# Kernel tuning notes

Hardware: AMD Instinct MI355X
Metric: run time of the kernel (lower is better)

## Reference

```python
import jax, jax.numpy as jnp
import numpy as np

HEADS = 8
DIM_HEAD = 64
DIM = 512
SCALE = DIM ** -0.5  # NOTE: original scales by dim**-0.5, not dim_head**-0.5


def setup_inputs() -> dict:
    key = jax.random.key(0)
    k1, k2, k3 = jax.random.split(key, 3)
    b, n = 2, 4096
    x = jax.random.normal(k1, (b, n, DIM), dtype=jnp.float32)
    Wqkv = jax.random.normal(k2, (DIM, 3 * HEADS * DIM_HEAD), dtype=jnp.float32) * (DIM ** -0.5)
    Wout = jax.random.normal(k3, (HEADS * DIM_HEAD, DIM), dtype=jnp.float32) * ((HEADS * DIM_HEAD) ** -0.5)
    b_out = jnp.zeros((DIM,), dtype=jnp.float32)
    return {"x": x, "Wqkv": Wqkv, "Wout": Wout, "b_out": b_out}


def reference(x, Wqkv, Wout, b_out):
    b, n, _ = x.shape
    h, d = HEADS, DIM_HEAD
    qkv = x @ Wqkv  # [b, n, 3*h*d]
    q, k, v = jnp.split(qkv, 3, axis=-1)
    to_heads = lambda t: t.reshape(b, n, h, d).transpose(0, 2, 1, 3)  # [b,h,n,d]
    q, k, v = to_heads(q), to_heads(k), to_heads(v)
    half = n // 2
    q_s, q_t = q[:, :, :half], q[:, :, half:]
    k_t = k[:, :, half:]  # k_s is unused in the original module
    v_s, v_t = v[:, :, :half], v[:, :, half:]
    # temporal branch: q_t attends to k_t, reads v_t
    dots_t = jnp.einsum('bhid,bhjd->bhij', q_t, k_t) * SCALE
    # spatial branch: cross-term q_s attends to k_t, reads v_s
    dots_s = jnp.einsum('bhid,bhjd->bhij', q_s, k_t) * SCALE
    attn_s = jax.nn.softmax(dots_s, axis=-1)
    attn_t = jax.nn.softmax(dots_t, axis=-1)
    out_s = jnp.einsum('bhij,bhjd->bhid', attn_s, v_s)
    out_t = jnp.einsum('bhij,bhjd->bhid', attn_t, v_t)
    out = jnp.concatenate([out_s, out_t], axis=2)  # [b,h,n,d]
    out = out.transpose(0, 2, 1, 3).reshape(b, n, h * d)
    return out @ Wout + b_out
```

## Files before the change

### kernel.cpp

```cpp
#include <hip/hip_runtime.h>
#include <hip/hip_bf16.h>

typedef __bf16 bf16;
typedef _Float16 f16;
typedef __bf16 bf16x4 __attribute__((ext_vector_type(4)));
typedef __bf16 bf16x8 __attribute__((ext_vector_type(8)));
typedef _Float16 f16x2 __attribute__((ext_vector_type(2)));
typedef _Float16 f16x4 __attribute__((ext_vector_type(4)));
typedef _Float16 f16x8 __attribute__((ext_vector_type(8)));
typedef float floatx4 __attribute__((ext_vector_type(4)));

static __device__ __forceinline__ floatx4 mfma_bf16(bf16x8 a, bf16x8 b, floatx4 c) {
  return __builtin_amdgcn_mfma_f32_16x16x32_bf16(a, b, c, 0, 0, 0);
}
static __device__ __forceinline__ floatx4 mfma_f16k32(f16x8 a, f16x8 b, floatx4 c) {
  return __builtin_amdgcn_mfma_f32_16x16x32_f16(a, b, c, 0, 0, 0);
}

static __device__ __forceinline__ void async16(void* lds, const void* gp) {
  __builtin_amdgcn_global_load_lds(
      (const __attribute__((address_space(1))) void*)gp,
      (__attribute__((address_space(3))) void*)lds, 16, 0, 0);
}

static __device__ __forceinline__ bf16x8 cvt8(float4 f0, float4 f1) {
  bf16x8 r;
  r[0] = (bf16)f0.x; r[1] = (bf16)f0.y; r[2] = (bf16)f0.z; r[3] = (bf16)f0.w;
  r[4] = (bf16)f1.x; r[5] = (bf16)f1.y; r[6] = (bf16)f1.z; r[7] = (bf16)f1.w;
  return r;
}

#define HEADS 8
#define DIMH 64
#define DIM 512
#define SEQ 4096
#define HALF 2048
#define BATCH 2
#define MROWS (BATCH * SEQ)
#define ELEMS ((size_t)MROWS * DIM)
#define NPARTS 4

#define C2F (0.044194173824159216f * 1.4426950408889634f)

__global__ __launch_bounds__(256)
void prep(const float* __restrict__ X, bf16* __restrict__ Xb,
          const float* __restrict__ wqkv, bf16* __restrict__ W1t,
          const float* __restrict__ wout, bf16* __restrict__ W2t) {
  __shared__ float tile[32][33];
  const int bid = blockIdx.x, t = threadIdx.x;
  if (bid < 2048) {
    size_t i = ((size_t)bid * 256 + t) * 8;
    float4 f0 = *reinterpret_cast<const float4*>(X + i);
    float4 f1 = *reinterpret_cast<const float4*>(X + i + 4);
    *reinterpret_cast<bf16x8*>(Xb + i) = cvt8(f0, f1);
    return;
  }
  const float* src; bf16* dst; int N, id;
  if (bid < 2816) { id = bid - 2048; src = wqkv; dst = W1t; N = 1536; }
  else            { id = bid - 2816; src = wout; dst = W2t; N = 512; }
  const int nb = N / 32;
  const int n0 = (id % nb) * 32, k0 = (id / nb) * 32;
  const int r = t >> 3, c4 = (t & 7) * 4;
  float4 v = *reinterpret_cast<const float4*>(src + (size_t)(k0 + r) * N + n0 + c4);
  tile[r][c4 + 0] = v.x; tile[r][c4 + 1] = v.y;
  tile[r][c4 + 2] = v.z; tile[r][c4 + 3] = v.w;
  __syncthreads();
  bf16x4 o;
#pragma unroll
  for (int i = 0; i < 4; ++i) o[i] = (bf16)tile[c4 + i][r];
  *reinterpret_cast<bf16x4*>(dst + (size_t)(n0 + r) * DIM + k0 + c4) = o;
}

__global__ __launch_bounds__(256)
void qkv_gemm(const bf16* __restrict__ Xb, const bf16* __restrict__ Wt,
              bf16* __restrict__ Qw, bf16* __restrict__ Kw, f16* __restrict__ Vt) {
  __shared__ __align__(16) char smem_raw[36864];

  const int m0 = blockIdx.x * 128, n0 = blockIdx.y * 128;
  const int t = threadIdx.x;
  const int wave = t >> 6, lane = t & 63, quad = lane >> 4, l16 = lane & 15;
  const int wr = wave >> 1, wc = wave & 1;

  f16 (*Ts)[72] = (f16(*)[72])(smem_raw + wave * 9216);

  floatx4 acc[4][4] = {};

  auto issue = [&](int buf, int k0) {
    bf16* Asf = (bf16*)(smem_raw + buf * 16384);
    bf16* Bsf = Asf + 4096;
#pragma unroll
    for (int it = 0; it < 2; ++it) {
      int g = it * 256 + t, row = g >> 2, c8 = (g & 3) * 8;
      async16(Asf + (size_t)g * 8, Xb + (size_t)(m0 + row) * DIM + k0 + c8);
      async16(Bsf + (size_t)g * 8, Wt + (size_t)(n0 + row) * DIM + k0 + c8);
    }
  };

  issue(0, 0);
  int buf = 0;
#pragma unroll 1
  for (int k0 = 0; k0 < DIM; k0 += 32) {
    __syncthreads();
    if (k0 + 32 < DIM) issue(buf ^ 1, k0 + 32);

    const bf16* Asf = (const bf16*)(smem_raw + buf * 16384);
    const bf16* Bsf = Asf + 4096;
    bf16x8 af[4], bfr[4];
#pragma unroll
    for (int mi = 0; mi < 4; ++mi)
      af[mi] = *reinterpret_cast<const bf16x8*>(
          Asf + (size_t)(wr * 64 + mi * 16 + l16) * 32 + quad * 8);
#pragma unroll
    for (int ni = 0; ni < 4; ++ni)
      bfr[ni] = *reinterpret_cast<const bf16x8*>(
          Bsf + (size_t)(wc * 64 + ni * 16 + l16) * 32 + quad * 8);
#pragma unroll
    for (int mi = 0; mi < 4; ++mi)
#pragma unroll
      for (int ni = 0; ni < 4; ++ni)
        acc[mi][ni] = mfma_bf16(af[mi], bfr[ni], acc[mi][ni]);
    buf ^= 1;
  }

  if (n0 < 1024) {
#pragma unroll
    for (int mi = 0; mi < 4; ++mi)
#pragma unroll
      for (int ni = 0; ni < 4; ++ni)
#pragma unroll
        for (int r = 0; r < 4; ++r) {
          int row = m0 + wr * 64 + mi * 16 + quad * 4 + r;
          int col = n0 + wc * 64 + ni * 16 + l16;
          int which = col >> 9, cc = col & 511;
          int head = cc >> 6, dim = cc & 63;
          int bb = row >> 12, nn = row & 4095;
          float val = acc[mi][ni][r];
          if (which == 0) val *= C2F;
          bf16* dst = which ? Kw : Qw;
          dst[(((size_t)(bb * HEADS + head)) * SEQ + nn) * DIMH + dim] = (bf16)val;
        }
  } else {
    __syncthreads();
    int head = (n0 + wc * 64 - 1024) >> 6;
#pragma unroll
    for (int mi = 0; mi < 4; ++mi)
#pragma unroll
      for (int ni = 0; ni < 4; ++ni) {
        f16x4 pv;
#pragma unroll
        for (int r = 0; r < 4; ++r) pv[r] = (f16)acc[mi][ni][r];
        *reinterpret_cast<f16x4*>(&Ts[ni * 16 + l16][mi * 16 + quad * 4]) = pv;
      }
    int bb = m0 >> 12, nnb = (m0 + wr * 64) & 4095;
    size_t base = ((size_t)(bb * HEADS + head)) * DIMH;
#pragma unroll
    for (int it = 0; it < 8; ++it) {
      int idx = lane + it * 64;
      int d = idx >> 3, ns = (idx & 7) * 8;
      *reinterpret_cast<f16x8*>(Vt + (base + d) * SEQ + nnb + ns) =
          *reinterpret_cast<const f16x8*>(&Ts[d][ns]);
    }
  }
}

__global__ __launch_bounds__(256)
void attn_kernel(const bf16* __restrict__ Q, const bf16* __restrict__ K,
                 const f16* __restrict__ Vt, f16* __restrict__ Opart,
                 float* __restrict__ Lpart) {
  __shared__ __align__(16) char smem[32768];

  const int bid = blockIdx.x;
  const int xcd = bid & 7, rem = bid >> 3;
  const int qt = rem & 31, ghi = rem >> 5;
  const int g = ghi * 8 + xcd;
  const int h = g >> 3, z = g & 7;
  const int bb = z >> 2, part = z & 3;

  const int t = threadIdx.x;
  const int wave = t >> 6, lane = t & 63, quad = lane >> 4, l16 = lane & 15;

  const size_t hb = ((size_t)(bb * HEADS + h)) * SEQ * DIMH;
  const int vhalf = (qt < 16) ? 0 : HALF;
  const int kstart = HALF + part * 512;
  const int vstart = vhalf + part * 512;
  const int q0 = qt * 128 + wave * 32;

  bf16x8 qa[2][2];
#pragma unroll
  for (int mt = 0; mt < 2; ++mt)
#pragma unroll
    for (int kc = 0; kc < 2; ++kc)
      qa[mt][kc] = *reinterpret_cast<const bf16x8*>(
          Q + hb + (size_t)(q0 + mt * 16 + l16) * DIMH + kc * 32 + quad * 8);

  floatx4 o_acc[2][4] = {};
  float l_acc[2] = {0.f, 0.f};

  const int r = t >> 3;
  const int rr = r & 15;
  const int kappa = (rr >> 2) * 8 + (rr & 3) + ((r & 16) ? 4 : 0);
  const int kchunk = (t & 7) ^ (r & 7);
  const bf16* kSrc = K + hb + (size_t)(kstart + kappa) * DIMH + kchunk * 8;

  const int vd = t >> 2;
  const int vchunk = (t & 3) ^ ((vd >> 1) & 3);
  const f16* vSrc = Vt + hb + (size_t)vd * SEQ + vstart + vchunk * 8;

  auto issue = [&](int slot, int kc0) {
    async16(smem + slot * 8192 + t * 16, kSrc + (size_t)kc0 * DIMH);
    async16(smem + slot * 8192 + 4096 + t * 16, vSrc + kc0);
  };

  const int koffA = l16 * 128 + ((quad ^ (l16 & 7)) * 16);
  const int voff = l16 * 64 + ((quad ^ ((l16 >> 1) & 3)) * 16);

  auto compute = [&](const char* Kb) {
    const char* Vb = Kb + 4096;
    __builtin_amdgcn_s_setprio(1);
    bf16x8 kaA0 = *reinterpret_cast<const bf16x8*>(Kb + koffA);
    bf16x8 kaA1 = *reinterpret_cast<const bf16x8*>(Kb + (koffA ^ 64));
    bf16x8 kaB0 = *reinterpret_cast<const bf16x8*>(Kb + 2048 + koffA);
    bf16x8 kaB1 = *reinterpret_cast<const bf16x8*>(Kb + 2048 + (koffA ^ 64));

    f16x8 pbm[2];
#pragma unroll
    for (int mt = 0; mt < 2; ++mt) {
      floatx4 stA = {0.f, 0.f, 0.f, 0.f}, stB = {0.f, 0.f, 0.f, 0.f};
      stA = mfma_bf16(kaA0, qa[mt][0], stA);
      stA = mfma_bf16(kaA1, qa[mt][1], stA);
      stB = mfma_bf16(kaB0, qa[mt][0], stB);
      stB = mfma_bf16(kaB1, qa[mt][1], stB);
      float ls = l_acc[mt];
      f16x8 pb;
#pragma unroll
      for (int rr2 = 0; rr2 < 4; ++rr2) {
        float pA = __builtin_amdgcn_exp2f(stA[rr2]);
        float pB = __builtin_amdgcn_exp2f(stB[rr2]);
        ls += pA + pB;
        pb[rr2] = (f16)pA;
        pb[4 + rr2] = (f16)pB;
      }
      l_acc[mt] = ls;
      pbm[mt] = pb;
    }
#pragma unroll
    for (int dsub = 0; dsub < 4; ++dsub) {
      f16x8 va = *reinterpret_cast<const f16x8*>(Vb + voff + dsub * 1024);
      o_acc[0][dsub] = mfma_f16k32(va, pbm[0], o_acc[0][dsub]);
      o_acc[1][dsub] = mfma_f16k32(va, pbm[1], o_acc[1][dsub]);
    }
    __builtin_amdgcn_s_setprio(0);
  };

  issue(0, 0);
  issue(1, 32);
  issue(2, 64);
#pragma unroll 1
  for (int i = 0; i < 16; ++i) {
    if (i <= 13)      asm volatile("s_waitcnt vmcnt(4)" ::: "memory");
    else if (i == 14) asm volatile("s_waitcnt vmcnt(2)" ::: "memory");
    else              asm volatile("s_waitcnt vmcnt(0)" ::: "memory");
    asm volatile("s_barrier" ::: "memory");
    if (i <= 12) issue((i + 3) & 3, (i + 3) * 32);
    compute(smem + (i & 3) * 8192);
  }

  f16* Op = Opart + (size_t)part * ELEMS;
  float* Lp = Lpart + (size_t)part * MROWS * HEADS;
#pragma unroll
  for (int mt = 0; mt < 2; ++mt) {
    float v = l_acc[mt];
    v += __shfl_xor(v, 16);
    v += __shfl_xor(v, 32);
    int n = q0 + mt * 16 + l16;
    size_t rowidx = (size_t)(bb * SEQ + n);
    if (quad == 0) Lp[rowidx * HEADS + h] = v;
    size_t rowbase = rowidx * DIM + h * DIMH;
#pragma unroll
    for (int dsub = 0; dsub < 4; ++dsub) {
      f16x4 ov;
#pragma unroll
      for (int r2 = 0; r2 < 4; ++r2) ov[r2] = (f16)o_acc[mt][dsub][r2];
      *reinterpret_cast<f16x4*>(Op + rowbase + dsub * 16 + quad * 4) = ov;
    }
  }
}

__global__ __launch_bounds__(256)
void out_gemm(const f16* __restrict__ Opart, const float* __restrict__ Lpart,
              const bf16* __restrict__ Wt, const float* __restrict__ bias,
              float* __restrict__ out) {
  __shared__ __align__(16) bf16 Asf[64 * 64];
  __shared__ __align__(16) bf16 Bsf[64 * 64];

  const int m0 = blockIdx.x * 64, n0 = blockIdx.y * 64;
  const int t = threadIdx.x;
  const int wave = t >> 6, lane = t & 63, quad = lane >> 4, l16 = lane & 15;
  const int m_off = (wave >> 1) * 32, n_off = (wave & 1) * 32;

  int srowi[2], sc8[2];
#pragma unroll
  for (int it = 0; it < 2; ++it) {
    int g = t + it * 256;
    srowi[it] = g >> 3; sc8[it] = (g & 7) * 8;
  }

  float linv[2][8];
#pragma unroll
  for (int it = 0; it < 2; ++it) {
    size_t ar = (size_t)(m0 + srowi[it]);
#pragma unroll
    for (int hh = 0; hh < 8; ++hh) {
      float s = 0.f;
#pragma unroll
      for (int p = 0; p < NPARTS; ++p)
        s += Lpart[(size_t)p * MROWS * HEADS + ar * HEADS + hh];
      linv[it][hh] = 1.0f / s;
    }
  }

  floatx4 acc[2][2] = {};

  f16x8 oreg[2][NPARTS];
  auto loadO = [&](int k0) {
#pragma unroll
    for (int it = 0; it < 2; ++it) {
      size_t abase = (size_t)(m0 + srowi[it]) * DIM + k0 + sc8[it];
#pragma unroll
      for (int p = 0; p < NPARTS; ++p)
        oreg[it][p] = *reinterpret_cast<const f16x8*>(Opart + (size_t)p * ELEMS + abase);
    }
  };

  loadO(0);
#pragma unroll 1
  for (int k0 = 0; k0 < DIM; k0 += 64) {
#pragma unroll
    for (int it = 0; it < 2; ++it) {
      int g = t + it * 256;
      async16(Bsf + (size_t)g * 8, Wt + (size_t)(n0 + srowi[it]) * DIM + k0 + sc8[it]);
      float inv = linv[it][(k0 + sc8[it]) >> 6];
      bf16x8 a;
#pragma unroll
      for (int j = 0; j < 8; ++j)
        a[j] = (bf16)(((float)oreg[it][0][j] + (float)oreg[it][1][j] +
                       (float)oreg[it][2][j] + (float)oreg[it][3][j]) * inv);
      *reinterpret_cast<bf16x8*>(Asf + (size_t)g * 8) = a;
    }
    __syncthreads();
    int nk = k0 + 64; if (nk >= DIM) nk = 0;
    loadO(nk);

#pragma unroll
    for (int kk = 0; kk < 2; ++kk) {
      bf16x8 a0 = *reinterpret_cast<const bf16x8*>(Asf + (size_t)(m_off + l16) * 64 + kk * 32 + quad * 8);
      bf16x8 a1 = *reinterpret_cast<const bf16x8*>(Asf + (size_t)(m_off + 16 + l16) * 64 + kk * 32 + quad * 8);
      bf16x8 b0 = *reinterpret_cast<const bf16x8*>(Bsf + (size_t)(n_off + l16) * 64 + kk * 32 + quad * 8);
      bf16x8 b1 = *reinterpret_cast<const bf16x8*>(Bsf + (size_t)(n_off + 16 + l16) * 64 + kk * 32 + quad * 8);
      acc[0][0] = mfma_bf16(a0, b0, acc[0][0]);
      acc[0][1] = mfma_bf16(a0, b1, acc[0][1]);
      acc[1][0] = mfma_bf16(a1, b0, acc[1][0]);
      acc[1][1] = mfma_bf16(a1, b1, acc[1][1]);
    }
    __syncthreads();
  }

#pragma unroll
  for (int mi = 0; mi < 2; ++mi)
#pragma unroll
    for (int ni = 0; ni < 2; ++ni)
#pragma unroll
      for (int r = 0; r < 4; ++r) {
        int row = m0 + m_off + mi * 16 + quad * 4 + r;
        int col = n0 + n_off + ni * 16 + l16;
        out[(size_t)row * DIM + col] = acc[mi][ni][r] + bias[col];
      }
}

extern "C" void kernel_launch(void* const* d_in, const int* in_sizes, int n_in,
                              void* d_out, int out_size, void* d_ws, size_t ws_size,
                              hipStream_t stream) {
  const float* x = (const float*)d_in[0];
  const float* wqkv = (const float*)d_in[1];
  const float* wout = (const float*)d_in[2];
  const float* bout = (const float*)d_in[3];
  float* out = (float*)d_out;

  char* ws = (char*)d_ws;
  f16* Opart = (f16*)ws;
  bf16* Xb = (bf16*)ws;
  bf16* Qw = (bf16*)(ws + ((size_t)32 << 20));
  bf16* Kw = Qw + ELEMS;
  f16* Vt = (f16*)(Kw + ELEMS);
  bf16* WtQKV = (bf16*)(Vt + ELEMS);
  bf16* WtOUT = WtQKV + (size_t)1536 * 512;
  float* Lpart = (float*)(WtOUT + (size_t)512 * 512);

  prep<<<3072, 256, 0, stream>>>(x, Xb, wqkv, WtQKV, wout, WtOUT);
  qkv_gemm<<<dim3(MROWS / 128, 1536 / 128), 256, 0, stream>>>(Xb, WtQKV, Qw, Kw, Vt);
  attn_kernel<<<2048, 256, 0, stream>>>(Qw, Kw, Vt, Opart, Lpart);
  out_gemm<<<dim3(MROWS / 64, DIM / 64), 256, 0, stream>>>(Opart, Lpart, WtOUT, bout, out);
}
```

Before: 156.2 us.

## Split attention into single-wave blocks with barrier-free double buffering and MFMA row sums

The attention kernel now runs one wave per block (8192 blocks of 64 threads) instead of four waves sharing K/V tiles. Each wave loads its own K/V tiles through a two-slot buffer and no longer needs s_barrier. The softmax row sum is computed by an MFMA against a ones vector in place of scalar adds and cross-lane shuffles. Dropping the barrier and the shuffles cuts synchronisation and VALU work, at the cost of four times the K/V global-to-LDS traffic, since tiles are no longer shared across waves, and a shallower prefetch depth.

Result: slower. 170.1 us (+8.9%).

```diff
diff --git a/kernel.cpp b/kernel.cpp
--- a/kernel.cpp
+++ b/kernel.cpp
@@ -163,27 +163,27 @@
   }
 }
 
-__global__ __launch_bounds__(256)
+__global__ __launch_bounds__(64, 4)
 void attn_kernel(const bf16* __restrict__ Q, const bf16* __restrict__ K,
                  const f16* __restrict__ Vt, f16* __restrict__ Opart,
                  float* __restrict__ Lpart) {
-  __shared__ __align__(16) char smem[32768];
+  __shared__ __align__(16) char smem[16384];
 
   const int bid = blockIdx.x;
   const int xcd = bid & 7, rem = bid >> 3;
-  const int qt = rem & 31, ghi = rem >> 5;
+  const int qw = rem & 127, ghi = rem >> 7;
   const int g = ghi * 8 + xcd;
   const int h = g >> 3, z = g & 7;
   const int bb = z >> 2, part = z & 3;
 
   const int t = threadIdx.x;
-  const int wave = t >> 6, lane = t & 63, quad = lane >> 4, l16 = lane & 15;
+  const int quad = t >> 4, l16 = t & 15;
 
   const size_t hb = ((size_t)(bb * HEADS + h)) * SEQ * DIMH;
-  const int vhalf = (qt < 16) ? 0 : HALF;
+  const int vhalf = (qw < 64) ? 0 : HALF;
   const int kstart = HALF + part * 512;
   const int vstart = vhalf + part * 512;
-  const int q0 = qt * 128 + wave * 32;
+  const int q0 = qw * 32;
 
   bf16x8 qa[2][2];
 #pragma unroll
@@ -194,25 +194,39 @@
           Q + hb + (size_t)(q0 + mt * 16 + l16) * DIMH + kc * 32 + quad * 8);
 
   floatx4 o_acc[2][4] = {};
-  float l_acc[2] = {0.f, 0.f};
-
-  const int r = t >> 3;
-  const int rr = r & 15;
-  const int kappa = (rr >> 2) * 8 + (rr & 3) + ((r & 16) ? 4 : 0);
-  const int kchunk = (t & 7) ^ (r & 7);
-  const bf16* kSrc = K + hb + (size_t)(kstart + kappa) * DIMH + kchunk * 8;
-
-  const int vd = t >> 2;
-  const int vchunk = (t & 3) ^ ((vd >> 1) & 3);
-  const f16* vSrc = Vt + hb + (size_t)vd * SEQ + vstart + vchunk * 8;
+  floatx4 lacc[2] = {};
+
+  const bf16* kSrcIt[4];
+#pragma unroll
+  for (int it = 0; it < 4; ++it) {
+    int g256 = it * 64 + t;
+    int r = g256 >> 3;
+    int rr = r & 15;
+    int kappa = (rr >> 2) * 8 + (rr & 3) + ((r & 16) ? 4 : 0);
+    int kchunk = (g256 & 7) ^ (r & 7);
+    kSrcIt[it] = K + hb + (size_t)(kstart + kappa) * DIMH + kchunk * 8;
+  }
+  const int vd0 = t >> 2;
+  const int vchunk = (t & 3) ^ ((vd0 >> 1) & 3);
+  const f16* vSrc = Vt + hb + (size_t)vd0 * SEQ + vstart + vchunk * 8;
 
   auto issue = [&](int slot, int kc0) {
-    async16(smem + slot * 8192 + t * 16, kSrc + (size_t)kc0 * DIMH);
-    async16(smem + slot * 8192 + 4096 + t * 16, vSrc + kc0);
+#pragma unroll
+    for (int it = 0; it < 4; ++it)
+      async16(smem + slot * 8192 + it * 1024 + t * 16,
+              kSrcIt[it] + (size_t)kc0 * DIMH);
+#pragma unroll
+    for (int it = 0; it < 4; ++it)
+      async16(smem + slot * 8192 + 4096 + it * 1024 + t * 16,
+              vSrc + kc0 + (size_t)(it * 16) * SEQ);
   };
 
   const int koffA = l16 * 128 + ((quad ^ (l16 & 7)) * 16);
   const int voff = l16 * 64 + ((quad ^ ((l16 >> 1) & 3)) * 16);
+
+  f16x8 ones;
+#pragma unroll
+  for (int j = 0; j < 8; ++j) ones[j] = (f16)1.0f;
 
   auto compute = [&](const char* Kb) {
     const char* Vb = Kb + 4096;
@@ -230,18 +244,14 @@
       stA = mfma_bf16(kaA1, qa[mt][1], stA);
       stB = mfma_bf16(kaB0, qa[mt][0], stB);
       stB = mfma_bf16(kaB1, qa[mt][1], stB);
-      float ls = l_acc[mt];
       f16x8 pb;
 #pragma unroll
       for (int rr2 = 0; rr2 < 4; ++rr2) {
-        float pA = __builtin_amdgcn_exp2f(stA[rr2]);
-        float pB = __builtin_amdgcn_exp2f(stB[rr2]);
-        ls += pA + pB;
-        pb[rr2] = (f16)pA;
-        pb[4 + rr2] = (f16)pB;
+        pb[rr2] = (f16)__builtin_amdgcn_exp2f(stA[rr2]);
+        pb[4 + rr2] = (f16)__builtin_amdgcn_exp2f(stB[rr2]);
       }
-      l_acc[mt] = ls;
       pbm[mt] = pb;
+      lacc[mt] = mfma_f16k32(ones, pb, lacc[mt]);
     }
 #pragma unroll
     for (int dsub = 0; dsub < 4; ++dsub) {
@@ -254,27 +264,32 @@
 
   issue(0, 0);
   issue(1, 32);
-  issue(2, 64);
 #pragma unroll 1
-  for (int i = 0; i < 16; ++i) {
-    if (i <= 13)      asm volatile("s_waitcnt vmcnt(4)" ::: "memory");
-    else if (i == 14) asm volatile("s_waitcnt vmcnt(2)" ::: "memory");
-    else              asm volatile("s_waitcnt vmcnt(0)" ::: "memory");
-    asm volatile("s_barrier" ::: "memory");
-    if (i <= 12) issue((i + 3) & 3, (i + 3) * 32);
-    compute(smem + (i & 3) * 8192);
+  for (int i = 0; i < 16; i += 2) {
+    asm volatile("s_waitcnt vmcnt(8)" ::: "memory");
+    compute(smem);
+    if (i + 2 < 16) {
+      asm volatile("s_waitcnt lgkmcnt(0)" ::: "memory");
+      __builtin_amdgcn_sched_barrier(0);
+      issue(0, (i + 2) * 32);
+    }
+    if (i + 1 == 15) asm volatile("s_waitcnt vmcnt(0)" ::: "memory");
+    else             asm volatile("s_waitcnt vmcnt(8)" ::: "memory");
+    compute(smem + 8192);
+    if (i + 3 < 16) {
+      asm volatile("s_waitcnt lgkmcnt(0)" ::: "memory");
+      __builtin_amdgcn_sched_barrier(0);
+      issue(1, (i + 3) * 32);
+    }
   }
 
   f16* Op = Opart + (size_t)part * ELEMS;
   float* Lp = Lpart + (size_t)part * MROWS * HEADS;
 #pragma unroll
   for (int mt = 0; mt < 2; ++mt) {
-    float v = l_acc[mt];
-    v += __shfl_xor(v, 16);
-    v += __shfl_xor(v, 32);
     int n = q0 + mt * 16 + l16;
     size_t rowidx = (size_t)(bb * SEQ + n);
-    if (quad == 0) Lp[rowidx * HEADS + h] = v;
+    if (quad == 0) Lp[rowidx * HEADS + h] = lacc[mt][0];
     size_t rowbase = rowidx * DIM + h * DIMH;
 #pragma unroll
     for (int dsub = 0; dsub < 4; ++dsub) {
@@ -398,6 +413,6 @@
 
   prep<<<3072, 256, 0, stream>>>(x, Xb, wqkv, WtQKV, wout, WtOUT);
   qkv_gemm<<<dim3(MROWS / 128, 1536 / 128), 256, 0, stream>>>(Xb, WtQKV, Qw, Kw, Vt);
-  attn_kernel<<<2048, 256, 0, stream>>>(Qw, Kw, Vt, Opart, Lpart);
+  attn_kernel<<<8192, 64, 0, stream>>>(Qw, Kw, Vt, Opart, Lpart);
   out_gemm<<<dim3(MROWS / 64, DIM / 64), 256, 0, stream>>>(Opart, Lpart, WtOUT, bout, out);
 }
```
